# Optimization experiments

Measured on AMD Instinct MI355X. Metric: run time of the kernel, lower is better.

## Reference

```python
import jax, jax.numpy as jnp
import numpy as np

N = 131072        # total nodes
D = 256           # d_model (params.emb_dim)
STEPS = 16        # depth steps
G = N // STEPS    # nodes per depth step (equal-sized groups)
B = 16            # batch (number of trees); all lengths equal N//B
V = 1024          # len(id2word)
# op schedule: -1 leaf embedding, -2 numeric encoder, 0/1 unary ('sin','cos'), 2/3 binary ('add','mul')
SCHEDULE = [-1, -2, 0, 2, 1, 3, 0, 2, 1, 3, 0, 2, 1, 3, 0, 2]


def setup_inputs() -> dict:
    key = jax.random.key(0)
    ks = jax.random.split(key, 8)
    tokens = jax.random.randint(ks[0], (N,), 0, V, dtype=jnp.int32)
    # children of a node at depth d must already be computed: indices < d*G
    rng = np.random.default_rng(0)
    li = np.zeros(N, np.int32)
    ri = np.zeros(N, np.int32)
    for d in range(2, STEPS):
        li[d * G:(d + 1) * G] = rng.integers(0, d * G, G)
        ri[d * G:(d + 1) * G] = rng.integers(0, d * G, G)
    depths = jnp.repeat(jnp.arange(STEPS, dtype=jnp.int32), G)
    operation_order = jnp.array(SCHEDULE, dtype=jnp.int32)
    lengths = jnp.full((B,), N // B, dtype=jnp.int32)
    s = 0.05
    leaf_table = jax.random.normal(ks[1], (V, D), jnp.float32)
    num_W1 = jax.random.normal(ks[2], (D, 1), jnp.float32) * s
    num_b1 = jnp.zeros((D,), jnp.float32)
    num_W2 = jax.random.normal(ks[3], (D, D), jnp.float32) * s
    num_b2 = jnp.zeros((D,), jnp.float32)
    una_W = jax.random.normal(ks[4], (2, 4, D, D), jnp.float32) * s
    una_b = jnp.zeros((2, 4, D), jnp.float32)
    bin_W = jax.random.normal(ks[5], (2, 10, D, D), jnp.float32) * s
    bin_b = jnp.zeros((2, 5, D), jnp.float32)
    return dict(tokens=tokens, left_idx=jnp.asarray(li), right_idx=jnp.asarray(ri),
                depths=depths, operation_order=operation_order, lengths=lengths,
                leaf_table=leaf_table, num_W1=num_W1, num_b1=num_b1,
                num_W2=num_W2, num_b2=num_b2,
                una_W=una_W, una_b=una_b, bin_W=bin_W, bin_b=bin_b)


def _unary_cell(hc, W, b):
    # hc: [G, 2, D]; W: [4, D, D] (data, forget, output, input); b: [4, D]
    h, c = hc[:, 0], hc[:, 1]
    g = jnp.einsum('nd,ked->kne', h, W) + b[:, None, :]  # y = h @ W_k.T + b_k
    i = jax.nn.sigmoid(g[0])
    f = jax.nn.sigmoid(g[1])
    o = jax.nn.sigmoid(g[2])
    u = jnp.tanh(g[3])
    c2 = i * u + f * c
    h2 = o * jnp.tanh(c2)
    h2 = h2 / jnp.linalg.norm(h2)  # global (Frobenius) norm, as in torch h.norm(p=2)
    c2 = c2 / jnp.linalg.norm(c2)
    return jnp.stack([h2, c2], axis=1)


def _binary_cell(hcl, hcr, W, b):
    # W: [10, D, D] = (data_l, data_r, f_ll, f_lr, f_rl, f_rr, out_l, out_r, in_l, in_r)
    # b: [5, D] = (data, forget_l, forget_r, output, input)
    hl, cl = hcl[:, 0], hcl[:, 1]
    hr, cr = hcr[:, 0], hcr[:, 1]
    gl = jnp.einsum('nd,ked->kne', hl, W[jnp.array([0, 2, 4, 6, 8])])
    gr = jnp.einsum('nd,ked->kne', hr, W[jnp.array([1, 3, 5, 7, 9])])
    g = gl + gr + b[:, None, :]
    i = jax.nn.sigmoid(g[0])
    f_l = jax.nn.sigmoid(g[1])
    f_r = jax.nn.sigmoid(g[2])
    o = jax.nn.sigmoid(g[3])
    u = jnp.tanh(g[4])
    c2 = i * u + f_l * cl + f_r * cr
    h2 = o * jnp.tanh(c2)
    h2 = h2 / jnp.linalg.norm(h2)
    c2 = c2 / jnp.linalg.norm(c2)
    return jnp.stack([h2, c2], axis=1)


def reference(tokens, left_idx, right_idx, depths, operation_order, lengths,
              leaf_table, num_W1, num_b1, num_W2, num_b2,
              una_W, una_b, bin_W, bin_b):
    sched = np.asarray(operation_order).tolist()  # static dispatch schedule
    n = tokens.shape[0]
    steps = len(sched)
    g = n // steps
    d_model = leaf_table.shape[1]
    acts = jnp.zeros((n, 2, d_model), leaf_table.dtype)
    for d, op in enumerate(sched):
        s = d * g
        if op == -1:  # leaf embedding with max_norm=1.0 renorm (non-differentiable scale)
            e = leaf_table[tokens[s:s + g]]
            nrm = jnp.linalg.norm(e, axis=-1, keepdims=True)
            scale = jax.lax.stop_gradient(jnp.minimum(1.0, 1.0 / (nrm + 1e-7)))
            e = e * scale
            step_act = jnp.stack([e, jnp.zeros_like(e)], axis=1)
        elif op == -2:  # numeric encoder
            x = tokens[s:s + g].astype(leaf_table.dtype)[:, None]
            h1 = jax.nn.sigmoid(x @ num_W1.T + num_b1)
            e = jax.nn.sigmoid(h1 @ num_W2.T + num_b2)
            step_act = jnp.stack([e, jnp.zeros_like(e)], axis=1)
        elif op in (0, 1):  # unary LSTM cell: gather child then cell
            child = acts[left_idx[s:s + g]]
            step_act = _unary_cell(child, una_W[op], una_b[op])
        else:  # binary LSTM cell: gather both children
            l = acts[left_idx[s:s + g]]
            r = acts[right_idx[s:s + g]]
            step_act = _binary_cell(l, r, bin_W[op - 2], bin_b[op - 2])
        acts = jax.lax.dynamic_update_slice(acts, step_act, (s, 0, 0))
    hidden = acts[:, 0, :]  # [N, D]
    batch = lengths.shape[0]
    # all lengths equal -> pad_sequence is a reshape: [B, L, D]
    return hidden.reshape(batch, n // batch, d_model)
```

## Files before the change

kernel.cpp:

```cpp
#include <hip/hip_runtime.h>
#include <hip/hip_bf16.h>
#include <cstdint>

typedef unsigned short u16;
typedef unsigned int u32;
typedef __attribute__((ext_vector_type(4))) float floatx4;
typedef __attribute__((ext_vector_type(8))) short shortx8;

#define G_STEP 8192
#define N_TOTAL 131072
#define RHALF (1280*256)

__device__ __forceinline__ float bfu2f(u16 x){ return __uint_as_float(((unsigned)x)<<16); }
__device__ __forceinline__ u16 f2bfu(float x){ __hip_bfloat16 b = __float2bfloat16(x); return *reinterpret_cast<u16*>(&b); }
__device__ __forceinline__ float sigm(float x){ return 1.0f/(1.0f+__expf(-x)); }
__device__ __forceinline__ float tanh_(float x){
  float cx = fminf(fmaxf(x,-15.f),15.f);
  float e = __expf(2.f*cx);
  return (e-1.f)/(e+1.f);
}
__device__ __forceinline__ float invs(float x){ return 1.0f/sqrtf(x); }

__device__ __forceinline__ void gl16(const void* g, void* l){
  __builtin_amdgcn_global_load_lds((const __attribute__((address_space(1))) u32*)g,
                                   (__attribute__((address_space(3))) u32*)l, 16, 0, 0);
}

__device__ __forceinline__ void cvt8(const float* __restrict__ src, u16* __restrict__ dst){
  float4 a = *reinterpret_cast<const float4*>(src);
  float4 b = *reinterpret_cast<const float4*>(src+4);
  ushort4 o0; o0.x=f2bfu(a.x); o0.y=f2bfu(a.y); o0.z=f2bfu(a.z); o0.w=f2bfu(a.w);
  ushort4 o1; o1.x=f2bfu(b.x); o1.y=f2bfu(b.y); o1.z=f2bfu(b.z); o1.w=f2bfu(b.w);
  *reinterpret_cast<ushort4*>(dst)   = o0;
  *reinterpret_cast<ushort4*>(dst+4) = o1;
}

__global__ __launch_bounds__(256) void setup_kernel(
    const int* __restrict__ tokens, const float* __restrict__ leaf_table,
    const float* __restrict__ W1, const float* __restrict__ b1,
    const float* __restrict__ una_W, const float* __restrict__ bin_W,
    const float* __restrict__ num_W2,
    u16* __restrict__ wbu, u16* __restrict__ wbb, u16* __restrict__ wbn,
    u16* __restrict__ h1, u16* __restrict__ H, u16* __restrict__ C,
    float* __restrict__ sumsq)
{
  const int b = blockIdx.x, tid = threadIdx.x;
  if (b < 256){
    int row = b*8 + (tid>>5), d0 = (tid&31)*8;
    int op = row>>10, w = row&1023;
    int gate = (w>>4)&3, e = ((w>>6)<<4) | (w&15);
    cvt8(una_W + (size_t)((op*4+gate)*256 + e)*256 + d0, wbu + (size_t)row*256 + d0);
  } else if (b < 896){
    int row = (b-256)*8 + (tid>>5), d0 = (tid&31)*8;
    int ob = row / 2560, rem = row - ob*2560;
    int lr = rem / 1280, rw = rem - lr*1280;
    int eblk = rw / 80, rem2 = rw - eblk*80;
    int gate = rem2 >> 4, el = rem2 & 15;
    int e = eblk*16 + el;
    cvt8(bin_W + (size_t)((ob*10 + 2*gate + lr)*256 + e)*256 + d0, wbb + (size_t)row*256 + d0);
  } else if (b < 928){
    int row = (b-896)*8 + (tid>>5), d0 = (tid&31)*8;
    cvt8(num_W2 + (size_t)row*256 + d0, wbn + (size_t)row*256 + d0);
  } else if (b < 2976){
    int wave = tid >> 6, lane = tid & 63;
    int node = (b-928)*4 + wave;
    int t = tokens[node];
    const float4 e4 = *reinterpret_cast<const float4*>(leaf_table + (size_t)t*256 + lane*4);
    float ss = e4.x*e4.x + e4.y*e4.y + e4.z*e4.z + e4.w*e4.w;
    #pragma unroll
    for (int o = 32; o; o >>= 1) ss += __shfl_down(ss, o);
    ss = __shfl(ss, 0);
    float scale = fminf(1.0f, 1.0f/(sqrtf(ss) + 1e-7f));
    ushort4 hv;
    hv.x = f2bfu(e4.x*scale); hv.y = f2bfu(e4.y*scale);
    hv.z = f2bfu(e4.z*scale); hv.w = f2bfu(e4.w*scale);
    ushort4 zv; zv.x = zv.y = zv.z = zv.w = 0;
    *reinterpret_cast<ushort4*>(H + (size_t)node*256 + lane*4) = hv;
    *reinterpret_cast<ushort4*>(C + (size_t)node*256 + lane*4) = zv;
  } else if (b < 4000){
    int flat = (b-2976)*2048 + tid*8;
    int n = flat >> 8, d0 = flat & 255;
    float x = (float)tokens[G_STEP + n];
    float4 w0 = *reinterpret_cast<const float4*>(W1 + d0);
    float4 w1 = *reinterpret_cast<const float4*>(W1 + d0 + 4);
    float4 c0 = *reinterpret_cast<const float4*>(b1 + d0);
    float4 c1 = *reinterpret_cast<const float4*>(b1 + d0 + 4);
    ushort4 o0, o1;
    o0.x = f2bfu(sigm(x*w0.x + c0.x)); o0.y = f2bfu(sigm(x*w0.y + c0.y));
    o0.z = f2bfu(sigm(x*w0.z + c0.z)); o0.w = f2bfu(sigm(x*w0.w + c0.w));
    o1.x = f2bfu(sigm(x*w1.x + c1.x)); o1.y = f2bfu(sigm(x*w1.y + c1.y));
    o1.z = f2bfu(sigm(x*w1.z + c1.z)); o1.w = f2bfu(sigm(x*w1.w + c1.w));
    *reinterpret_cast<ushort4*>(h1 + flat)     = o0;
    *reinterpret_cast<ushort4*>(h1 + flat + 4) = o1;
  } else {
    if (tid < 32) sumsq[tid] = ((tid & 15) < 2) ? 1.0f : 0.0f;
  }
}

template<int MODE>
__global__ __launch_bounds__(256, 2) void gemm_fused(
    const u16* __restrict__ Asrc, const int* __restrict__ lidx,
    const int* __restrict__ ridx, const u16* __restrict__ Wb,
    const float* __restrict__ bias, const u16* __restrict__ Cin,
    float* __restrict__ sumsq, u16* __restrict__ H, u16* __restrict__ C,
    int sbase, int step)
{
  constexpr int NG  = (MODE==0) ? 1 : (MODE==1 ? 4 : 5);
  constexpr int NBR = (MODE==2) ? 160 : 128;
  constexpr int NT  = (MODE==2) ? 8 : 4;
  constexpr int BR  = NBR/32;
  constexpr int WN  = (MODE==2) ? 80 : 64;
  constexpr int NFR = WN/16;

  __shared__ u16 SA[2][128][64];
  __shared__ u16 SB[2][NBR][64];
  __shared__ float scC[16];
  __shared__ float red[8];

  const int tid  = threadIdx.x;
  const int lane = tid & 63, wave = tid >> 6;
  const int mbase = blockIdx.x*128;
  const int nbase = blockIdx.y*NBR;
  const int l15 = lane & 15, kg = lane >> 4;
  const int rhi = lane >> 3;
  const int lc  = (lane & 7) ^ rhi;

  if (MODE != 0 && tid < 16) scC[tid] = invs(sumsq[16 + tid]);

  const u16* aL[4]; const u16* aR[4]; const u16* bP[BR];
  #pragma unroll
  for (int rr = 0; rr < 4; rr++){
    int r = rr*32 + wave*8 + rhi;
    int gr;
    if constexpr (MODE==0) gr = mbase + r;
    else                   gr = lidx[sbase + mbase + r];
    aL[rr] = Asrc + (size_t)gr*256 + lc*8;
    if constexpr (MODE==2)
      aR[rr] = Asrc + (size_t)ridx[sbase + mbase + r]*256 + lc*8;
  }
  #pragma unroll
  for (int rb = 0; rb < BR; rb++){
    int r = rb*32 + wave*8 + rhi;
    bP[rb] = Wb + (size_t)(nbase + r)*256 + lc*8;
  }

  floatx4 acc[4][NFR];
  #pragma unroll
  for (int i = 0; i < 4; i++)
    #pragma unroll
    for (int j = 0; j < NFR; j++) acc[i][j] = (floatx4)(0.0f);

  const int wm = (wave >> 1)*64, wn = (wave & 1)*WN;

  auto stage = [&](int t, int buf){
    const int kk = t*64;
    #pragma unroll
    for (int rr = 0; rr < 4; rr++){
      const u16* ga;
      if constexpr (MODE==2){ ga = (kk >= 256) ? aR[rr] + (kk-256) : aL[rr] + kk; }
      else                  { ga = aL[rr] + kk; }
      gl16(ga, &SA[buf][rr*32 + wave*8][0]);
    }
    #pragma unroll
    for (int rb = 0; rb < BR; rb++){
      const u16* gb;
      if constexpr (MODE==2){ gb = (kk >= 256) ? bP[rb] + RHALF + (kk-256) : bP[rb] + kk; }
      else                  { gb = bP[rb] + kk; }
      gl16(gb, &SB[buf][rb*32 + wave*8][0]);
    }
  };

  stage(0, 0);
  __syncthreads();

  #pragma unroll
  for (int t = 0; t < NT; t++){
    if (t+1 < NT) stage(t+1, (t+1)&1);
    const int buf = t & 1;
    #pragma unroll
    for (int j = 0; j < 2; j++){
      shortx8 af[4], bfr[NFR];
      const int pc = ((j*4 + kg) ^ (l15 & 7)) * 8;
      #pragma unroll
      for (int i = 0; i < 4; i++)
        af[i] = *reinterpret_cast<const shortx8*>(&SA[buf][wm + i*16 + l15][pc]);
      #pragma unroll
      for (int n = 0; n < NFR; n++)
        bfr[n] = *reinterpret_cast<const shortx8*>(&SB[buf][wn + n*16 + l15][pc]);
      #pragma unroll
      for (int mi = 0; mi < 4; mi++)
        #pragma unroll
        for (int ni = 0; ni < NFR; ni++)
          acc[mi][ni] = __builtin_amdgcn_mfma_f32_16x16x32_bf16(af[mi], bfr[ni], acc[mi][ni], 0, 0, 0);
    }
    __syncthreads();
  }

  if constexpr (MODE == 0){
    float bb[4];
    #pragma unroll
    for (int ni = 0; ni < 4; ni++) bb[ni] = bias[nbase + wn + ni*16 + l15];
    #pragma unroll
    for (int mi = 0; mi < 4; mi++){
      #pragma unroll
      for (int r = 0; r < 4; r++){
        int node = sbase + mbase + wm + mi*16 + kg*4 + r;
        u16* hp = H + (size_t)node*256 + nbase + wn + l15;
        u16* cp = C + (size_t)node*256 + nbase + wn + l15;
        #pragma unroll
        for (int ni = 0; ni < 4; ni++){
          hp[ni*16] = f2bfu(sigm(acc[mi][ni][r] + bb[ni]));
          cp[ni*16] = 0;
        }
      }
    }
  } else {
    const int eb = blockIdx.y*2 + (wave & 1);
    const int e  = eb*16 + l15;
    float bb[NG];
    #pragma unroll
    for (int g = 0; g < NG; g++) bb[g] = bias[g*256 + e];
    float hss = 0.f, css = 0.f;
    #pragma unroll
    for (int mi = 0; mi < 4; mi++){
      #pragma unroll
      for (int r = 0; r < 4; r++){
        int orow = mbase + wm + mi*16 + kg*4 + r;
        int node = sbase + orow;
        int chl = lidx[node];
        float cl = bfu2f(Cin[(size_t)chl*256 + e]) * scC[chl >> 13];
        float c2, h2;
        if constexpr (MODE == 1){
          float i_ = sigm(acc[mi][0][r] + bb[0]);
          float f_ = sigm(acc[mi][1][r] + bb[1]);
          float o_ = sigm(acc[mi][2][r] + bb[2]);
          float u_ = tanh_(acc[mi][3][r] + bb[3]);
          c2 = i_*u_ + f_*cl;
          h2 = o_*tanh_(c2);
        } else {
          int chr = ridx[node];
          float cr = bfu2f(Cin[(size_t)chr*256 + e]) * scC[chr >> 13];
          float i_ = sigm(acc[mi][0][r] + bb[0]);
          float fl = sigm(acc[mi][1][r] + bb[1]);
          float fr = sigm(acc[mi][2][r] + bb[2]);
          float o_ = sigm(acc[mi][3][r] + bb[3]);
          float u_ = tanh_(acc[mi][4][r] + bb[4]);
          c2 = i_*u_ + fl*cl + fr*cr;
          h2 = o_*tanh_(c2);
        }
        H[(size_t)node*256 + e] = f2bfu(h2);
        C[(size_t)node*256 + e] = f2bfu(c2);
        hss += h2*h2;
        css += c2*c2;
      }
    }
    #pragma unroll
    for (int o = 32; o; o >>= 1){ hss += __shfl_down(hss, o); css += __shfl_down(css, o); }
    if (lane == 0){ red[wave] = hss; red[4+wave] = css; }
    __syncthreads();
    if (tid == 0)  atomicAdd(&sumsq[step],      red[0]+red[1]+red[2]+red[3]);
    if (tid == 64) atomicAdd(&sumsq[16 + step], red[4]+red[5]+red[6]+red[7]);
  }
}

__global__ __launch_bounds__(256) void norm_h_kernel(
    u16* __restrict__ H, const float* __restrict__ sumsq, int step)
{
  float s = invs(sumsq[step]);
  size_t base = (size_t)step*G_STEP*256 + ((size_t)blockIdx.x*256 + threadIdx.x)*8;
  uint4 v = *reinterpret_cast<const uint4*>(H + base);
  uint4 o;
  #define MUL2(p) ( (u32)f2bfu(bfu2f((u16)((p)&0xffff))*s) | ((u32)f2bfu(bfu2f((u16)((p)>>16))*s) << 16) )
  o.x = MUL2(v.x); o.y = MUL2(v.y); o.z = MUL2(v.z); o.w = MUL2(v.w);
  #undef MUL2
  *reinterpret_cast<uint4*>(H + base) = o;
}

__global__ __launch_bounds__(256) void out_kernel(
    const u16* __restrict__ H, const float* __restrict__ sumsq, float* __restrict__ out)
{
  size_t base = ((size_t)blockIdx.x*256 + threadIdx.x)*8;
  int n = (int)(base >> 8);
  float s = ((n >> 13) == 15) ? invs(sumsq[15]) : 1.0f;
  const uint4 v = *reinterpret_cast<const uint4*>(H + base);
  float4 o0, o1;
  o0.x = bfu2f((u16)(v.x & 0xffff))*s; o0.y = bfu2f((u16)(v.x >> 16))*s;
  o0.z = bfu2f((u16)(v.y & 0xffff))*s; o0.w = bfu2f((u16)(v.y >> 16))*s;
  o1.x = bfu2f((u16)(v.z & 0xffff))*s; o1.y = bfu2f((u16)(v.z >> 16))*s;
  o1.z = bfu2f((u16)(v.w & 0xffff))*s; o1.w = bfu2f((u16)(v.w >> 16))*s;
  *reinterpret_cast<float4*>(out + base)     = o0;
  *reinterpret_cast<float4*>(out + base + 4) = o1;
}

extern "C" void kernel_launch(void* const* d_in, const int* in_sizes, int n_in,
                              void* d_out, int out_size, void* d_ws, size_t ws_size,
                              hipStream_t stream)
{
  const int*   tokens     = (const int*)d_in[0];
  const int*   lidx       = (const int*)d_in[1];
  const int*   ridx       = (const int*)d_in[2];
  const float* leaf_table = (const float*)d_in[6];
  const float* num_W1     = (const float*)d_in[7];
  const float* num_b1     = (const float*)d_in[8];
  const float* num_W2     = (const float*)d_in[9];
  const float* num_b2     = (const float*)d_in[10];
  const float* una_W      = (const float*)d_in[11];
  const float* una_b      = (const float*)d_in[12];
  const float* bin_W      = (const float*)d_in[13];
  const float* bin_b      = (const float*)d_in[14];

  char* ws = (char*)d_ws;
  size_t off = 0;
  u16* H   = (u16*)(ws + off); off += (size_t)N_TOTAL*256*2;
  u16* wbu = (u16*)(ws + off); off += (size_t)2048*256*2;
  u16* wbb = (u16*)(ws + off); off += (size_t)5120*256*2;
  u16* wbn = (u16*)(ws + off); off += (size_t)256*256*2;
  u16* h1  = (u16*)(ws + off); off += (size_t)G_STEP*256*2;
  float* sumsq = (float*)(ws + off); off += 32*4;

  u16* C = (u16*)d_out;

  setup_kernel<<<4001, 256, 0, stream>>>(tokens, leaf_table, num_W1, num_b1,
                                         una_W, bin_W, num_W2,
                                         wbu, wbb, wbn, h1, H, C, sumsq);
  gemm_fused<0><<<dim3(64, 2), 256, 0, stream>>>(
      h1, nullptr, nullptr, wbn, num_b2, nullptr, sumsq, H, C, G_STEP, 1);

  const int sched[16] = {-1,-2,0,2,1,3,0,2,1,3,0,2,1,3,0,2};
  for (int d = 2; d < 16; d++){
    int op = sched[d];
    int sbase = d*G_STEP;
    if (op == 0 || op == 1){
      gemm_fused<1><<<dim3(64, 8), 256, 0, stream>>>(
          H, lidx, nullptr, wbu + (size_t)op*1024*256,
          una_b + (size_t)op*4*256, C, sumsq, H, C, sbase, d);
    } else {
      int o2 = op - 2;
      gemm_fused<2><<<dim3(64, 8), 256, 0, stream>>>(
          H, lidx, ridx, wbb + (size_t)o2*2*1280*256,
          bin_b + (size_t)o2*5*256, C, sumsq, H, C, sbase, d);
    }
    if (d < 15) norm_h_kernel<<<1024, 256, 0, stream>>>(H, sumsq, d);
  }
  out_kernel<<<(N_TOTAL*256)/(256*8), 256, 0, stream>>>(H, sumsq, (float*)d_out);
}
```

Measured before the change: 399.9 us.

## Fold hidden-state norm scaling into GEMM epilogues and drop norm_h kernel

Removes the per-step norm_h_kernel that rescaled each step's H in place. Stored H now stays unnormalised, and each consumer applies the per-step inverse norm to the GEMM result. The binary cell keeps separate left and right accumulators so each child's scale can be applied in the epilogue, and out_kernel scales every step. This saves 13 launches and a read-modify-write pass over H per step. In exchange it doubles accumulator registers in the binary kernel, which risks occupancy or spills.

```diff
diff --git a/kernel.cpp b/kernel.cpp
--- a/kernel.cpp
+++ b/kernel.cpp
@@ -114,6 +114,7 @@
 
   __shared__ u16 SA[2][128][64];
   __shared__ u16 SB[2][NBR][64];
+  __shared__ float scH[16];
   __shared__ float scC[16];
   __shared__ float red[8];
 
@@ -125,7 +126,10 @@
   const int rhi = lane >> 3;
   const int lc  = (lane & 7) ^ rhi;
 
-  if (MODE != 0 && tid < 16) scC[tid] = invs(sumsq[16 + tid]);
+  if (MODE != 0){
+    if (tid < 16)           scH[tid]    = invs(sumsq[tid]);
+    else if (tid < 32)      scC[tid-16] = invs(sumsq[tid]);
+  }
 
   const u16* aL[4]; const u16* aR[4]; const u16* bP[BR];
   #pragma unroll
@@ -144,11 +148,18 @@
     bP[rb] = Wb + (size_t)(nbase + r)*256 + lc*8;
   }
 
-  floatx4 acc[4][NFR];
+  floatx4 accL[4][NFR];
   #pragma unroll
   for (int i = 0; i < 4; i++)
     #pragma unroll
-    for (int j = 0; j < NFR; j++) acc[i][j] = (floatx4)(0.0f);
+    for (int j = 0; j < NFR; j++) accL[i][j] = (floatx4)(0.0f);
+  floatx4 accR[(MODE==2)?4:1][(MODE==2)?NFR:1];
+  if constexpr (MODE==2){
+    #pragma unroll
+    for (int i = 0; i < 4; i++)
+      #pragma unroll
+      for (int j = 0; j < NFR; j++) accR[i][j] = (floatx4)(0.0f);
+  }
 
   const int wm = (wave >> 1)*64, wn = (wave & 1)*WN;
 
@@ -187,11 +198,19 @@
       #pragma unroll
       for (int n = 0; n < NFR; n++)
         bfr[n] = *reinterpret_cast<const shortx8*>(&SB[buf][wn + n*16 + l15][pc]);
-      #pragma unroll
-      for (int mi = 0; mi < 4; mi++)
+      if (MODE==2 && t >= 4){
         #pragma unroll
-        for (int ni = 0; ni < NFR; ni++)
-          acc[mi][ni] = __builtin_amdgcn_mfma_f32_16x16x32_bf16(af[mi], bfr[ni], acc[mi][ni], 0, 0, 0);
+        for (int mi = 0; mi < 4; mi++)
+          #pragma unroll
+          for (int ni = 0; ni < NFR; ni++)
+            accR[mi][ni] = __builtin_amdgcn_mfma_f32_16x16x32_bf16(af[mi], bfr[ni], accR[mi][ni], 0, 0, 0);
+      } else {
+        #pragma unroll
+        for (int mi = 0; mi < 4; mi++)
+          #pragma unroll
+          for (int ni = 0; ni < NFR; ni++)
+            accL[mi][ni] = __builtin_amdgcn_mfma_f32_16x16x32_bf16(af[mi], bfr[ni], accL[mi][ni], 0, 0, 0);
+      }
     }
     __syncthreads();
   }
@@ -209,7 +228,7 @@
         u16* cp = C + (size_t)node*256 + nbase + wn + l15;
         #pragma unroll
         for (int ni = 0; ni < 4; ni++){
-          hp[ni*16] = f2bfu(sigm(acc[mi][ni][r] + bb[ni]));
+          hp[ni*16] = f2bfu(sigm(accL[mi][ni][r] + bb[ni]));
           cp[ni*16] = 0;
         }
       }
@@ -228,23 +247,30 @@
         int orow = mbase + wm + mi*16 + kg*4 + r;
         int node = sbase + orow;
         int chl = lidx[node];
+        float sl = scH[chl >> 13];
         float cl = bfu2f(Cin[(size_t)chl*256 + e]) * scC[chl >> 13];
         float c2, h2;
         if constexpr (MODE == 1){
-          float i_ = sigm(acc[mi][0][r] + bb[0]);
-          float f_ = sigm(acc[mi][1][r] + bb[1]);
-          float o_ = sigm(acc[mi][2][r] + bb[2]);
-          float u_ = tanh_(acc[mi][3][r] + bb[3]);
+          float i_ = sigm(accL[mi][0][r]*sl + bb[0]);
+          float f_ = sigm(accL[mi][1][r]*sl + bb[1]);
+          float o_ = sigm(accL[mi][2][r]*sl + bb[2]);
+          float u_ = tanh_(accL[mi][3][r]*sl + bb[3]);
           c2 = i_*u_ + f_*cl;
           h2 = o_*tanh_(c2);
         } else {
           int chr = ridx[node];
+          float sr = scH[chr >> 13];
           float cr = bfu2f(Cin[(size_t)chr*256 + e]) * scC[chr >> 13];
-          float i_ = sigm(acc[mi][0][r] + bb[0]);
-          float fl = sigm(acc[mi][1][r] + bb[1]);
-          float fr = sigm(acc[mi][2][r] + bb[2]);
-          float o_ = sigm(acc[mi][3][r] + bb[3]);
-          float u_ = tanh_(acc[mi][4][r] + bb[4]);
+          float g0 = accL[mi][0][r]*sl + accR[mi][0][r]*sr + bb[0];
+          float g1 = accL[mi][1][r]*sl + accR[mi][1][r]*sr + bb[1];
+          float g2 = accL[mi][2][r]*sl + accR[mi][2][r]*sr + bb[2];
+          float g3 = accL[mi][3][r]*sl + accR[mi][3][r]*sr + bb[3];
+          float g4 = accL[mi][4][r]*sl + accR[mi][4][r]*sr + bb[4];
+          float i_ = sigm(g0);
+          float fl = sigm(g1);
+          float fr = sigm(g2);
+          float o_ = sigm(g3);
+          float u_ = tanh_(g4);
           c2 = i_*u_ + fl*cl + fr*cr;
           h2 = o_*tanh_(c2);
         }
@@ -263,25 +289,12 @@
   }
 }
 
-__global__ __launch_bounds__(256) void norm_h_kernel(
-    u16* __restrict__ H, const float* __restrict__ sumsq, int step)
-{
-  float s = invs(sumsq[step]);
-  size_t base = (size_t)step*G_STEP*256 + ((size_t)blockIdx.x*256 + threadIdx.x)*8;
-  uint4 v = *reinterpret_cast<const uint4*>(H + base);
-  uint4 o;
-  #define MUL2(p) ( (u32)f2bfu(bfu2f((u16)((p)&0xffff))*s) | ((u32)f2bfu(bfu2f((u16)((p)>>16))*s) << 16) )
-  o.x = MUL2(v.x); o.y = MUL2(v.y); o.z = MUL2(v.z); o.w = MUL2(v.w);
-  #undef MUL2
-  *reinterpret_cast<uint4*>(H + base) = o;
-}
-
 __global__ __launch_bounds__(256) void out_kernel(
     const u16* __restrict__ H, const float* __restrict__ sumsq, float* __restrict__ out)
 {
   size_t base = ((size_t)blockIdx.x*256 + threadIdx.x)*8;
   int n = (int)(base >> 8);
-  float s = ((n >> 13) == 15) ? invs(sumsq[15]) : 1.0f;
+  float s = invs(sumsq[n >> 13]);
   const uint4 v = *reinterpret_cast<const uint4*>(H + base);
   float4 o0, o1;
   o0.x = bfu2f((u16)(v.x & 0xffff))*s; o0.y = bfu2f((u16)(v.x >> 16))*s;
@@ -340,7 +353,6 @@
           H, lidx, ridx, wbb + (size_t)o2*2*1280*256,
           bin_b + (size_t)o2*5*256, C, sumsq, H, C, sbase, d);
     }
-    if (d < 15) norm_h_kernel<<<1024, 256, 0, stream>>>(H, sumsq, d);
   }
   out_kernel<<<(N_TOTAL*256)/(256*8), 256, 0, stream>>>(H, sumsq, (float*)d_out);
 }
```

After: 381.7 us. -4.5%, faster.

## Fold H normalization into GEMM epilogue and shrink tiles with deeper pipelining

Applied to the files above, without the earlier changes.

Removes the per-step norm_h_kernel pass. The child-H norm scale is now applied inside the GEMM: the unary cell scales its accumulators, and the binary cell rescales partial sums between its left and right halves (sl/sr). out_kernel then applies the per-step scale to every row. The GEMM tile drops to 64 rows with K-chunks of 32, uses a two-stage prefetch managed by explicit vmcnt/lgkmcnt waits, and raises occupancy to 4 blocks per CU. In exchange, rounding changes because unnormalized bf16 H is kept, and the hand-tuned waitcnt sequence is fragile.

```diff
diff --git a/kernel.cpp b/kernel.cpp
--- a/kernel.cpp
+++ b/kernel.cpp
@@ -25,6 +25,12 @@
   __builtin_amdgcn_global_load_lds((const __attribute__((address_space(1))) u32*)g,
                                    (__attribute__((address_space(3))) u32*)l, 16, 0, 0);
 }
+
+template<int V> __device__ __forceinline__ void wait_vm();
+template<> __device__ __forceinline__ void wait_vm<0>(){ asm volatile("s_waitcnt vmcnt(0)" ::: "memory"); }
+template<> __device__ __forceinline__ void wait_vm<3>(){ asm volatile("s_waitcnt vmcnt(3)" ::: "memory"); }
+template<> __device__ __forceinline__ void wait_vm<4>(){ asm volatile("s_waitcnt vmcnt(4)" ::: "memory"); }
+__device__ __forceinline__ void wait_lgkm0(){ asm volatile("s_waitcnt lgkmcnt(0)" ::: "memory"); }
 
 __device__ __forceinline__ void cvt8(const float* __restrict__ src, u16* __restrict__ dst){
   float4 a = *reinterpret_cast<const float4*>(src);
@@ -98,7 +104,7 @@
 }
 
 template<int MODE>
-__global__ __launch_bounds__(256, 2) void gemm_fused(
+__global__ __launch_bounds__(256, 4) void gemm_fused(
     const u16* __restrict__ Asrc, const int* __restrict__ lidx,
     const int* __restrict__ ridx, const u16* __restrict__ Wb,
     const float* __restrict__ bias, const u16* __restrict__ Cin,
@@ -107,93 +113,122 @@
 {
   constexpr int NG  = (MODE==0) ? 1 : (MODE==1 ? 4 : 5);
   constexpr int NBR = (MODE==2) ? 160 : 128;
-  constexpr int NT  = (MODE==2) ? 8 : 4;
-  constexpr int BR  = NBR/32;
+  constexpr int NT  = (MODE==2) ? 16 : 8;
   constexpr int WN  = (MODE==2) ? 80 : 64;
   constexpr int NFR = WN/16;
-
-  __shared__ u16 SA[2][128][64];
-  __shared__ u16 SB[2][NBR][64];
+  constexpr int NBI = (MODE==2) ? 3 : 2;
+
+  __shared__ u16 SA[2][64][32];
+  __shared__ u16 SB[2][NBR][32];
+  __shared__ float scH[16];
   __shared__ float scC[16];
   __shared__ float red[8];
 
   const int tid  = threadIdx.x;
   const int lane = tid & 63, wave = tid >> 6;
-  const int mbase = blockIdx.x*128;
+  const int mbase = blockIdx.x*64;
   const int nbase = blockIdx.y*NBR;
   const int l15 = lane & 15, kg = lane >> 4;
-  const int rhi = lane >> 3;
-  const int lc  = (lane & 7) ^ rhi;
-
-  if (MODE != 0 && tid < 16) scC[tid] = invs(sumsq[16 + tid]);
-
-  const u16* aL[4]; const u16* aR[4]; const u16* bP[BR];
+  const int srow = lane >> 2;
+  const int sch  = (lane & 3) ^ (srow & 3);
+  const int wm = (wave >> 1)*32, wn = (wave & 1)*WN;
+
+  if (MODE != 0){
+    if (tid < 16)      scH[tid]    = invs(sumsq[tid]);
+    else if (tid < 32) scC[tid-16] = invs(sumsq[tid]);
+  }
+
+  int chl_[2][4], chr_[2][4];
+  if constexpr (MODE != 0){
+    #pragma unroll
+    for (int mi = 0; mi < 2; mi++)
+      #pragma unroll
+      for (int r = 0; r < 4; r++){
+        int node = sbase + mbase + wm + mi*16 + kg*4 + r;
+        chl_[mi][r] = lidx[node];
+        if constexpr (MODE==2) chr_[mi][r] = ridx[node];
+      }
+  }
+
+  const u16* aL; const u16* aR = nullptr;
+  {
+    int r = mbase + wave*16 + srow;
+    int gr;
+    if constexpr (MODE==0) gr = r; else gr = lidx[sbase + r];
+    aL = Asrc + (size_t)gr*256 + sch*8;
+    if constexpr (MODE==2) aR = Asrc + (size_t)ridx[sbase + r]*256 + sch*8;
+  }
+  const int bstart = (MODE==2) ? (wave < 2 ? wave*3 : wave + 4) : wave*2;
+  const u16* bptr0 = Wb + (size_t)(nbase + bstart*16 + srow)*256 + sch*8;
+
+  __builtin_amdgcn_sched_barrier(0);
+
+  floatx4 acc[2][NFR];
   #pragma unroll
-  for (int rr = 0; rr < 4; rr++){
-    int r = rr*32 + wave*8 + rhi;
-    int gr;
-    if constexpr (MODE==0) gr = mbase + r;
-    else                   gr = lidx[sbase + mbase + r];
-    aL[rr] = Asrc + (size_t)gr*256 + lc*8;
-    if constexpr (MODE==2)
-      aR[rr] = Asrc + (size_t)ridx[sbase + mbase + r]*256 + lc*8;
-  }
-  #pragma unroll
-  for (int rb = 0; rb < BR; rb++){
-    int r = rb*32 + wave*8 + rhi;
-    bP[rb] = Wb + (size_t)(nbase + r)*256 + lc*8;
-  }
-
-  floatx4 acc[4][NFR];
-  #pragma unroll
-  for (int i = 0; i < 4; i++)
+  for (int i = 0; i < 2; i++)
     #pragma unroll
     for (int j = 0; j < NFR; j++) acc[i][j] = (floatx4)(0.0f);
 
-  const int wm = (wave >> 1)*64, wn = (wave & 1)*WN;
-
   auto stage = [&](int t, int buf){
-    const int kk = t*64;
-    #pragma unroll
-    for (int rr = 0; rr < 4; rr++){
-      const u16* ga;
-      if constexpr (MODE==2){ ga = (kk >= 256) ? aR[rr] + (kk-256) : aL[rr] + kk; }
-      else                  { ga = aL[rr] + kk; }
-      gl16(ga, &SA[buf][rr*32 + wave*8][0]);
-    }
-    #pragma unroll
-    for (int rb = 0; rb < BR; rb++){
-      const u16* gb;
-      if constexpr (MODE==2){ gb = (kk >= 256) ? bP[rb] + RHALF + (kk-256) : bP[rb] + kk; }
-      else                  { gb = bP[rb] + kk; }
-      gl16(gb, &SB[buf][rb*32 + wave*8][0]);
+    const bool rh = (MODE==2) && (t >= 8);
+    const int kk = rh ? (t-8)*32 : t*32;
+    const u16* ga = (rh ? aR : aL) + kk;
+    gl16(ga, &SA[buf][wave*16][0]);
+    #pragma unroll
+    for (int i = 0; i < NBI; i++){
+      const u16* gb = bptr0 + i*4096 + kk + (rh ? RHALF : 0);
+      gl16(gb, &SB[buf][(bstart + i)*16][0]);
     }
   };
 
   stage(0, 0);
-  __syncthreads();
+  stage(1, 1);
+  if constexpr (MODE==2) asm volatile("s_waitcnt vmcnt(4) lgkmcnt(0)" ::: "memory");
+  else                   asm volatile("s_waitcnt vmcnt(3) lgkmcnt(0)" ::: "memory");
+  __builtin_amdgcn_s_barrier();
 
   #pragma unroll
   for (int t = 0; t < NT; t++){
-    if (t+1 < NT) stage(t+1, (t+1)&1);
     const int buf = t & 1;
-    #pragma unroll
-    for (int j = 0; j < 2; j++){
-      shortx8 af[4], bfr[NFR];
-      const int pc = ((j*4 + kg) ^ (l15 & 7)) * 8;
+    shortx8 af[2], bfr[NFR];
+    const int pc = (kg ^ (l15 & 3)) * 8;
+    #pragma unroll
+    for (int i = 0; i < 2; i++)
+      af[i] = *reinterpret_cast<const shortx8*>(&SA[buf][wm + i*16 + l15][pc]);
+    #pragma unroll
+    for (int n = 0; n < NFR; n++)
+      bfr[n] = *reinterpret_cast<const shortx8*>(&SB[buf][wn + n*16 + l15][pc]);
+    wait_lgkm0();
+    __builtin_amdgcn_s_barrier();
+    if (t + 2 < NT) stage(t+2, buf);
+
+    if constexpr (MODE==2){
+      if (t == 8){
+        #pragma unroll
+        for (int mi = 0; mi < 2; mi++)
+          #pragma unroll
+          for (int r = 0; r < 4; r++){
+            float sl = scH[chl_[mi][r] >> 13];
+            float sr = scH[chr_[mi][r] >> 13];
+            float k = sl / sr;
+            #pragma unroll
+            for (int ni = 0; ni < NFR; ni++) acc[mi][ni][r] *= k;
+          }
+      }
+    }
+
+    #pragma unroll
+    for (int mi = 0; mi < 2; mi++)
       #pragma unroll
-      for (int i = 0; i < 4; i++)
-        af[i] = *reinterpret_cast<const shortx8*>(&SA[buf][wm + i*16 + l15][pc]);
-      #pragma unroll
-      for (int n = 0; n < NFR; n++)
-        bfr[n] = *reinterpret_cast<const shortx8*>(&SB[buf][wn + n*16 + l15][pc]);
-      #pragma unroll
-      for (int mi = 0; mi < 4; mi++)
-        #pragma unroll
-        for (int ni = 0; ni < NFR; ni++)
-          acc[mi][ni] = __builtin_amdgcn_mfma_f32_16x16x32_bf16(af[mi], bfr[ni], acc[mi][ni], 0, 0, 0);
-    }
-    __syncthreads();
+      for (int ni = 0; ni < NFR; ni++)
+        acc[mi][ni] = __builtin_amdgcn_mfma_f32_16x16x32_bf16(af[mi], bfr[ni], acc[mi][ni], 0, 0, 0);
+
+    if (t + 1 < NT){
+      if (t + 2 < NT){
+        if constexpr (MODE==2) wait_vm<4>(); else wait_vm<3>();
+      } else wait_vm<0>();
+      __builtin_amdgcn_s_barrier();
+    }
   }
 
   if constexpr (MODE == 0){
@@ -201,7 +236,7 @@
     #pragma unroll
     for (int ni = 0; ni < 4; ni++) bb[ni] = bias[nbase + wn + ni*16 + l15];
     #pragma unroll
-    for (int mi = 0; mi < 4; mi++){
+    for (int mi = 0; mi < 2; mi++){
       #pragma unroll
       for (int r = 0; r < 4; r++){
         int node = sbase + mbase + wm + mi*16 + kg*4 + r;
@@ -222,29 +257,30 @@
     for (int g = 0; g < NG; g++) bb[g] = bias[g*256 + e];
     float hss = 0.f, css = 0.f;
     #pragma unroll
-    for (int mi = 0; mi < 4; mi++){
+    for (int mi = 0; mi < 2; mi++){
       #pragma unroll
       for (int r = 0; r < 4; r++){
-        int orow = mbase + wm + mi*16 + kg*4 + r;
-        int node = sbase + orow;
-        int chl = lidx[node];
+        int node = sbase + mbase + wm + mi*16 + kg*4 + r;
+        int chl = chl_[mi][r];
         float cl = bfu2f(Cin[(size_t)chl*256 + e]) * scC[chl >> 13];
         float c2, h2;
         if constexpr (MODE == 1){
-          float i_ = sigm(acc[mi][0][r] + bb[0]);
-          float f_ = sigm(acc[mi][1][r] + bb[1]);
-          float o_ = sigm(acc[mi][2][r] + bb[2]);
-          float u_ = tanh_(acc[mi][3][r] + bb[3]);
+          float sl = scH[chl >> 13];
+          float i_ = sigm(acc[mi][0][r]*sl + bb[0]);
+          float f_ = sigm(acc[mi][1][r]*sl + bb[1]);
+          float o_ = sigm(acc[mi][2][r]*sl + bb[2]);
+          float u_ = tanh_(acc[mi][3][r]*sl + bb[3]);
           c2 = i_*u_ + f_*cl;
           h2 = o_*tanh_(c2);
         } else {
-          int chr = ridx[node];
+          int chr = chr_[mi][r];
+          float sr = scH[chr >> 13];
           float cr = bfu2f(Cin[(size_t)chr*256 + e]) * scC[chr >> 13];
-          float i_ = sigm(acc[mi][0][r] + bb[0]);
-          float fl = sigm(acc[mi][1][r] + bb[1]);
-          float fr = sigm(acc[mi][2][r] + bb[2]);
-          float o_ = sigm(acc[mi][3][r] + bb[3]);
-          float u_ = tanh_(acc[mi][4][r] + bb[4]);
+          float i_ = sigm(acc[mi][0][r]*sr + bb[0]);
+          float fl = sigm(acc[mi][1][r]*sr + bb[1]);
+          float fr = sigm(acc[mi][2][r]*sr + bb[2]);
+          float o_ = sigm(acc[mi][3][r]*sr + bb[3]);
+          float u_ = tanh_(acc[mi][4][r]*sr + bb[4]);
           c2 = i_*u_ + fl*cl + fr*cr;
           h2 = o_*tanh_(c2);
         }
@@ -263,25 +299,12 @@
   }
 }
 
-__global__ __launch_bounds__(256) void norm_h_kernel(
-    u16* __restrict__ H, const float* __restrict__ sumsq, int step)
-{
-  float s = invs(sumsq[step]);
-  size_t base = (size_t)step*G_STEP*256 + ((size_t)blockIdx.x*256 + threadIdx.x)*8;
-  uint4 v = *reinterpret_cast<const uint4*>(H + base);
-  uint4 o;
-  #define MUL2(p) ( (u32)f2bfu(bfu2f((u16)((p)&0xffff))*s) | ((u32)f2bfu(bfu2f((u16)((p)>>16))*s) << 16) )
-  o.x = MUL2(v.x); o.y = MUL2(v.y); o.z = MUL2(v.z); o.w = MUL2(v.w);
-  #undef MUL2
-  *reinterpret_cast<uint4*>(H + base) = o;
-}
-
 __global__ __launch_bounds__(256) void out_kernel(
     const u16* __restrict__ H, const float* __restrict__ sumsq, float* __restrict__ out)
 {
   size_t base = ((size_t)blockIdx.x*256 + threadIdx.x)*8;
   int n = (int)(base >> 8);
-  float s = ((n >> 13) == 15) ? invs(sumsq[15]) : 1.0f;
+  float s = invs(sumsq[n >> 13]);
   const uint4 v = *reinterpret_cast<const uint4*>(H + base);
   float4 o0, o1;
   o0.x = bfu2f((u16)(v.x & 0xffff))*s; o0.y = bfu2f((u16)(v.x >> 16))*s;
@@ -323,7 +346,7 @@
   setup_kernel<<<4001, 256, 0, stream>>>(tokens, leaf_table, num_W1, num_b1,
                                          una_W, bin_W, num_W2,
                                          wbu, wbb, wbn, h1, H, C, sumsq);
-  gemm_fused<0><<<dim3(64, 2), 256, 0, stream>>>(
+  gemm_fused<0><<<dim3(128, 2), 256, 0, stream>>>(
       h1, nullptr, nullptr, wbn, num_b2, nullptr, sumsq, H, C, G_STEP, 1);
 
   const int sched[16] = {-1,-2,0,2,1,3,0,2,1,3,0,2,1,3,0,2};
@@ -331,16 +354,15 @@
     int op = sched[d];
     int sbase = d*G_STEP;
     if (op == 0 || op == 1){
-      gemm_fused<1><<<dim3(64, 8), 256, 0, stream>>>(
+      gemm_fused<1><<<dim3(128, 8), 256, 0, stream>>>(
           H, lidx, nullptr, wbu + (size_t)op*1024*256,
           una_b + (size_t)op*4*256, C, sumsq, H, C, sbase, d);
     } else {
       int o2 = op - 2;
-      gemm_fused<2><<<dim3(64, 8), 256, 0, stream>>>(
+      gemm_fused<2><<<dim3(128, 8), 256, 0, stream>>>(
           H, lidx, ridx, wbb + (size_t)o2*2*1280*256,
           bin_b + (size_t)o2*5*256, C, sumsq, H, C, sbase, d);
     }
-    if (d < 15) norm_h_kernel<<<1024, 256, 0, stream>>>(H, sumsq, d);
   }
   out_kernel<<<(N_TOTAL*256)/(256*8), 256, 0, stream>>>(H, sumsq, (float*)d_out);
 }
```

Result: slower. 472.9 us (+18.3%).
